# Kernel optimization log

Hardware: AMD Instinct MI355X
Metric: run time of the kernel (lower is better)

The kernel has to match this reference:

```python
import jax, jax.numpy as jnp
import numpy as np
from jax import lax

D_TEMPORAL, D_INNER, D_STATE, D_CONV, DT_RANK = 2, 4, 16, 4, 1
EPS = 1e-5


def setup_inputs() -> dict:
    key = jax.random.key(0)
    ks = jax.random.split(key, 14)
    B, L = 16, 32768
    f = lambda k, s, scale=1.0: jax.random.normal(k, s, jnp.float32) * scale
    dt_b = float(np.log(np.expm1(0.01)))  # softplus^-1(0.01), typical dt init
    A_log = jnp.log(jnp.tile(jnp.arange(1, D_STATE + 1, dtype=jnp.float32), (D_INNER, 1)))
    return {
        "hidden_states": f(ks[0], (B, D_TEMPORAL, L)),
        "norm_w": jnp.ones((D_TEMPORAL,), jnp.float32),
        "in_proj_w": f(ks[1], (2 * D_INNER, D_TEMPORAL), 0.5),
        "conv_w": f(ks[2], (D_INNER, D_CONV), 0.3),
        "conv_b": f(ks[3], (D_INNER,), 0.1),
        "x_proj_w": f(ks[4], (DT_RANK + 2 * D_STATE, D_INNER), 0.3),
        "dt_proj_w": f(ks[5], (D_INNER, DT_RANK), 1.0),
        "dt_proj_b": jnp.full((D_INNER,), dt_b, jnp.float32),
        "A_log": A_log,
        "D": jnp.ones((D_INNER,), jnp.float32),
        "conv_w_b": f(ks[6], (D_INNER, D_CONV), 0.3),
        "conv_b_b": f(ks[7], (D_INNER,), 0.1),
        "x_proj_w_b": f(ks[8], (DT_RANK + 2 * D_STATE, D_INNER), 0.3),
        "dt_proj_w_b": f(ks[9], (D_INNER, DT_RANK), 1.0),
        "dt_proj_b_b": jnp.full((D_INNER,), dt_b, jnp.float32),
        "A_b_log": A_log,
        "D_b": jnp.ones((D_INNER,), jnp.float32),
        "out_proj_w": f(ks[10], (D_TEMPORAL, D_INNER), 0.3),
        "norm_f_w": jnp.ones((D_TEMPORAL,), jnp.float32),
    }


def _silu(x):
    return x * jax.nn.sigmoid(x)


def _rmsnorm(x, w):
    return x * lax.rsqrt(jnp.mean(x * x, axis=-1, keepdims=True) + EPS) * w


def _branch(x, z, conv_w, conv_b, x_proj_w, dt_proj_w, dt_proj_b, A_log, D):
    # x, z: (B, d_inner, L). Causal depthwise conv + silu.
    Bb, d, L = x.shape
    xc = lax.conv_general_dilated(
        x, conv_w[:, None, :], (1,), [(D_CONV - 1, 0)],
        feature_group_count=d, dimension_numbers=("NCH", "OIH", "NCH"))
    u = _silu(xc + conv_b[None, :, None]).transpose(0, 2, 1)      # (B, L, d)
    x_dbl = u @ x_proj_w.T                                        # (B, L, rank+2n)
    dt, Bm, Cm = jnp.split(x_dbl, [DT_RANK, DT_RANK + D_STATE], axis=-1)
    dt = jax.nn.softplus(dt @ dt_proj_w.T + dt_proj_b)            # (B, L, d)
    A = -jnp.exp(A_log)                                           # (d, n)
    dA = jnp.exp(dt[..., None] * A)                               # (B, L, d, n)
    dBu = (dt * u)[..., None] * Bm[:, :, None, :]                 # (B, L, d, n)

    def step(h, inp):
        dA_t, dBu_t, C_t = inp
        h = dA_t * h + dBu_t                                      # (B, d, n)
        return h, jnp.einsum("bdn,bn->bd", h, C_t)

    h0 = jnp.zeros((Bb, d, D_STATE), dtype=u.dtype)
    _, ys = lax.scan(step, h0, (jnp.swapaxes(dA, 0, 1), jnp.swapaxes(dBu, 0, 1), jnp.swapaxes(Cm, 0, 1)))
    y = jnp.swapaxes(ys, 0, 1) + u * D                            # (B, L, d)
    return y * _silu(z.transpose(0, 2, 1))


def _forward(hidden_states, norm_w, in_proj_w, conv_w, conv_b, x_proj_w, dt_proj_w,
             dt_proj_b, A_log, D, conv_w_b, conv_b_b, x_proj_w_b, dt_proj_w_b,
             dt_proj_b_b, A_b_log, D_b, out_proj_w, norm_f_w):
    # hidden_states: (B, T=d_temporal, L); scan runs over L.
    hs = jnp.swapaxes(hidden_states, 1, 2)                        # (B, L, T)
    residual = hs.astype(jnp.float32)
    hs = _rmsnorm(residual, norm_w)
    xz = jnp.swapaxes(hs @ in_proj_w.T, 1, 2)                     # (B, 2*d_inner, L)
    x, z = jnp.split(xz, 2, axis=1)
    y_f = _branch(x, z, conv_w, conv_b, x_proj_w, dt_proj_w, dt_proj_b, A_log, D)
    y_b = _branch(x[..., ::-1], z[..., ::-1], conv_w_b, conv_b_b, x_proj_w_b,
                  dt_proj_w_b, dt_proj_b_b, A_b_log, D_b)
    y = y_f + y_b[:, ::-1, :]                                     # (B, L, d_inner)
    out = y @ out_proj_w.T                                        # (B, L, T)
    out = _rmsnorm(out + residual, norm_f_w)
    return jnp.swapaxes(out, 1, 2)                                # (B, T, L)


def reference(hidden_states, norm_w, in_proj_w, conv_w, conv_b, x_proj_w, dt_proj_w,
              dt_proj_b, A_log, D, conv_w_b, conv_b_b, x_proj_w_b, dt_proj_w_b,
              dt_proj_b_b, A_b_log, D_b, out_proj_w, norm_f_w):
    return _forward(hidden_states, norm_w, in_proj_w, conv_w, conv_b, x_proj_w,
                    dt_proj_w, dt_proj_b, A_log, D, conv_w_b, conv_b_b, x_proj_w_b,
                    dt_proj_w_b, dt_proj_b_b, A_b_log, D_b, out_proj_w, norm_f_w)
```

## Files before the change

### kernel.cpp

```cpp
#include <hip/hip_runtime.h>
#include <cstdint>

#define BB 16
#define LL 32768
#define NC 512
#define NSPAN 32
#define SPLEN 16
#define CPG 8

#define WD_SZ 256
#define XPW 0
#define CVW 132
#define CVB 148
#define DTW 152
#define DTB 156
#define AW  160
#define DW  224
#define G_INPROJ 512
#define G_NORMW 528
#define G_OUTP 530
#define G_NORMF 538
#define FLG 1000

#define PQ_OFF 4096
#define PQ_BYTES ((size_t)BB*2*NC*64*8)
#define SP_OFF (PQ_OFF + PQ_BYTES)
#define SP_BYTES ((size_t)BB*2*NSPAN*64*8)
#define WG_OFF (SP_OFF + SP_BYTES)
#define WG_BYTES ((size_t)BB*NC*2*64*64*2)
#define YB_OFF (WG_OFF + WG_BYTES)
#define YB_BYTES ((size_t)BB*NC*64*4*4)

#define LOG2E 1.4426950408889634f

__device__ __forceinline__ float bf2f(unsigned short u){ return __uint_as_float(((unsigned int)u)<<16); }
__device__ __forceinline__ float blo(unsigned int u){ return __uint_as_float(u<<16); }
__device__ __forceinline__ float bhi(unsigned int u){ return __uint_as_float(u & 0xffff0000u); }

__device__ __forceinline__ unsigned int cvtpk(float lo, float hi){
  unsigned int r;
  asm("v_cvt_pk_bf16_f32 %0, %1, %2" : "=v"(r) : "v"(lo), "v"(hi));
  return r;
}
__device__ __forceinline__ unsigned short cvt1(float x){
  return (unsigned short)cvtpk(x, x);
}

__device__ __forceinline__ float siluf(float x){ return x / (1.f + __expf(-x)); }
__device__ __forceinline__ float softplusf_(float x){ return fmaxf(x,0.f) + log1pf(__expf(-fabsf(x))); }

__device__ __forceinline__ float exp2fast(float x){
#if __has_builtin(__builtin_amdgcn_exp2f)
  return __builtin_amdgcn_exp2f(x);
#else
  float r; asm("v_exp_f32 %0, %1\ns_nop 0" : "=v"(r) : "v"(x)); return r;
#endif
}

__device__ __forceinline__ float rowsum16(float x){
  asm("s_nop 1\n\t"
      "v_add_f32_dpp %0, %0, %0 row_ror:1 row_mask:0xf bank_mask:0xf\n\t"
      "s_nop 1\n\t"
      "v_add_f32_dpp %0, %0, %0 row_ror:2 row_mask:0xf bank_mask:0xf\n\t"
      "s_nop 1\n\t"
      "v_add_f32_dpp %0, %0, %0 row_ror:4 row_mask:0xf bank_mask:0xf\n\t"
      "s_nop 1\n\t"
      "v_add_f32_dpp %0, %0, %0 row_ror:8 row_mask:0xf bank_mask:0xf"
      : "+v"(x));
  return x;
}

__device__ __forceinline__ float ldw(const void* p, int i, int isf){
  return isf ? ((const float*)p)[i] : bf2f(((const unsigned short*)p)[i]);
}
__device__ __forceinline__ float2 hid2(const void* hid, int isf, int b, int t){
  if (isf){
    const float* p = (const float*)hid;
    return make_float2(p[(size_t)b*2*LL + t], p[(size_t)b*2*LL + LL + t]);
  }
  const unsigned short* p = (const unsigned short*)hid;
  return make_float2(bf2f(p[(size_t)b*2*LL + t]), bf2f(p[(size_t)b*2*LL + LL + t]));
}
__device__ __forceinline__ float4 xrow(const void* __restrict__ hid, int isf,
                                       const float* __restrict__ W, int b, int t){
  float2 h = hid2(hid, isf, b, t);
  float ms = rsqrtf(0.5f*(h.x*h.x + h.y*h.y) + 1e-5f);
  float v0 = h.x*ms*W[G_NORMW], v1 = h.y*ms*W[G_NORMW+1];
  float4 x;
  x.x = W[G_INPROJ+0]*v0 + W[G_INPROJ+1]*v1;
  x.y = W[G_INPROJ+2]*v0 + W[G_INPROJ+3]*v1;
  x.z = W[G_INPROJ+4]*v0 + W[G_INPROJ+5]*v1;
  x.w = W[G_INPROJ+6]*v0 + W[G_INPROJ+7]*v1;
  return x;
}

__global__ void k_prep(const void* __restrict__ normw, const void* __restrict__ inpj,
    const void* __restrict__ cwf, const void* __restrict__ cbf,
    const void* __restrict__ xpf, const void* __restrict__ dwf,
    const void* __restrict__ dbf, const void* __restrict__ alf,
    const void* __restrict__ ddf,
    const void* __restrict__ cwb, const void* __restrict__ cbb,
    const void* __restrict__ xpb, const void* __restrict__ dwb,
    const void* __restrict__ dbb, const void* __restrict__ alb,
    const void* __restrict__ ddb,
    const void* __restrict__ outp, const void* __restrict__ nfw,
    float* __restrict__ W)
{
  const int isf = (((const unsigned int*)ddf)[0] == 0x3F800000u) ? 1 : 0;
  int t = threadIdx.x;
  for (int i=t;i<132;i+=256){ W[XPW+i]=ldw(xpf,i,isf); W[WD_SZ+XPW+i]=ldw(xpb,i,isf); }
  for (int i=t;i<16;i+=256){ W[CVW+i]=ldw(cwf,i,isf); W[WD_SZ+CVW+i]=ldw(cwb,i,isf); W[G_INPROJ+i]=ldw(inpj,i,isf); }
  for (int i=t;i<4;i+=256){
    W[CVB+i]=ldw(cbf,i,isf); W[WD_SZ+CVB+i]=ldw(cbb,i,isf);
    W[DTW+i]=ldw(dwf,i,isf); W[WD_SZ+DTW+i]=ldw(dwb,i,isf);
    W[DTB+i]=ldw(dbf,i,isf); W[WD_SZ+DTB+i]=ldw(dbb,i,isf);
    W[DW+i] =ldw(ddf,i,isf); W[WD_SZ+DW+i] =ldw(ddb,i,isf);
  }
  for (int i=t;i<64;i+=256){
    W[AW+i]       = -__expf(ldw(alf,i,isf)) * LOG2E;
    W[WD_SZ+AW+i] = -__expf(ldw(alb,i,isf)) * LOG2E;
  }
  for (int i=t;i<8;i+=256) W[G_OUTP+i]=ldw(outp,i,isf);
  for (int i=t;i<2;i+=256){ W[G_NORMW+i]=ldw(normw,i,isf); W[G_NORMF+i]=ldw(nfw,i,isf); }
  if (t==0) W[FLG] = (float)isf;
}

template<int DR>
__device__ __forceinline__ float2 scan_store(const float (* __restrict__ dtPd)[68],
    const unsigned short (* __restrict__ dtud)[68],
    const unsigned int (* __restrict__ bcd)[68],
    float (* __restrict__ ySd)[68],
    unsigned short* __restrict__ wrow,
    float Ax, int d, int n, int dn)
{
  unsigned short* wr   = wrow + dn;
  unsigned short* wrHi = wr + 32*64;
  float P = 1.f, h = 0.f;
  for (int j4=0; j4<16; j4++){
    const int t0 = DR ? 60-4*j4 : 4*j4;
    float4  d4 = *(const float4*)&dtPd[d][t0];
    ushort4 u4 = *(const ushort4*)&dtud[d][t0];
    uint4   c4 = *(const uint4*)&bcd[n][t0];
    float da[4]={d4.x,d4.y,d4.z,d4.w};
    unsigned short ua[4]={u4.x,u4.y,u4.z,u4.w};
    unsigned int ca[4]={c4.x,c4.y,c4.z,c4.w};
    float s[4];
    #pragma unroll
    for (int jr=0; jr<4; jr++){
      const int k  = DR ? 3-jr : jr;
      const int tt = t0 + k;
      float e = exp2fast(Ax*da[k]);
      P *= e;
      float Cf = bhi(ca[k]);
      h = fmaf(e, h, bf2f(ua[k])*blo(ca[k]));
      ((tt < 32) ? wr : wrHi)[(tt & 31)*64] = cvt1(P*Cf);
      s[k] = rowsum16(h*Cf);
    }
    if (n == 0) *(float4*)&ySd[d][t0] = make_float4(s[0],s[1],s[2],s[3]);
  }
  return make_float2(P, h);
}

__global__ __launch_bounds__(128, 4) void k_chunk2(const void* __restrict__ hid,
    const float* __restrict__ W, float2* __restrict__ PQ,
    unsigned short* __restrict__ Wg, float4* __restrict__ YB)
{
  __shared__ __align__(16) char smx[2176];
  __shared__ __align__(16) float dtP[2][4][68];
  __shared__ __align__(16) unsigned short dtuP[2][4][68];
  __shared__ __align__(16) unsigned int BCp[2][16][68];
  __shared__ __align__(16) float uD[2][256];
  float4* xb = (float4*)smx;
  float (*yS)[4][68] = (float (*)[4][68])smx;

  const int tid  = threadIdx.x;
  const int wid  = tid >> 6;
  const int lane = tid & 63;
  const int gid  = blockIdx.x;
  const int c    = gid & (NC-1);
  const int b    = gid >> 9;
  const int isf  = (int)W[FLG];

  if (wid == 0){
    int t = c*64 + lane;
    xb[lane+3] = xrow(hid, isf, W, b, t);
    if (lane < 3){
      int t2 = c*64 - 3 + lane;
      float4 v = make_float4(0.f,0.f,0.f,0.f);
      if (t2 >= 0) v = xrow(hid, isf, W, b, t2);
      xb[lane] = v;
    }
    if (lane >= 61){
      int t3 = c*64 + lane + 3;
      float4 v = make_float4(0.f,0.f,0.f,0.f);
      if (t3 < LL) v = xrow(hid, isf, W, b, t3);
      xb[lane+6] = v;
    }
  }
  __syncthreads();
  {
    const float* Wd = W + wid*WD_SZ;
    float4 a0,a1,a2,a3;
    if (wid == 0){ a0=xb[lane];   a1=xb[lane+1]; a2=xb[lane+2]; a3=xb[lane+3]; }
    else         { a0=xb[lane+6]; a1=xb[lane+5]; a2=xb[lane+4]; a3=xb[lane+3]; }
    float u[4];
    u[0] = siluf(Wd[CVB+0] + Wd[CVW+ 0]*a0.x + Wd[CVW+ 1]*a1.x + Wd[CVW+ 2]*a2.x + Wd[CVW+ 3]*a3.x);
    u[1] = siluf(Wd[CVB+1] + Wd[CVW+ 4]*a0.y + Wd[CVW+ 5]*a1.y + Wd[CVW+ 6]*a2.y + Wd[CVW+ 7]*a3.y);
    u[2] = siluf(Wd[CVB+2] + Wd[CVW+ 8]*a0.z + Wd[CVW+ 9]*a1.z + Wd[CVW+10]*a2.z + Wd[CVW+11]*a3.z);
    u[3] = siluf(Wd[CVB+3] + Wd[CVW+12]*a0.w + Wd[CVW+13]*a1.w + Wd[CVW+14]*a2.w + Wd[CVW+15]*a3.w);
    float dtr = Wd[XPW+0]*u[0] + Wd[XPW+1]*u[1] + Wd[XPW+2]*u[2] + Wd[XPW+3]*u[3];
    float4 ud4;
    #pragma unroll
    for (int d2=0; d2<4; d2++){
      float dt = softplusf_(fmaf(Wd[DTW+d2], dtr, Wd[DTB+d2]));
      dtP[wid][d2][lane]  = dt;
      dtuP[wid][d2][lane] = cvt1(dt*u[d2]);
      ((float*)&ud4)[d2] = u[d2]*Wd[DW+d2];
    }
    *(float4*)&uD[wid][lane*4] = ud4;
    #pragma unroll
    for (int n=0; n<16; n++){
      float Bn = Wd[XPW+(1+n)*4+0]*u[0] + Wd[XPW+(1+n)*4+1]*u[1]
               + Wd[XPW+(1+n)*4+2]*u[2] + Wd[XPW+(1+n)*4+3]*u[3];
      float Cn = Wd[XPW+(17+n)*4+0]*u[0] + Wd[XPW+(17+n)*4+1]*u[1]
               + Wd[XPW+(17+n)*4+2]*u[2] + Wd[XPW+(17+n)*4+3]*u[3];
      BCp[wid][n][lane] = cvtpk(Bn, Cn);
    }
  }
  __syncthreads();

  const int d = lane>>4, n = lane&15;
  const float Ax = W[wid*WD_SZ + AW + d*16 + n];
  unsigned short* wrow = Wg + ((size_t)gid*2 + wid)*64*64;
  float2 pq;
  size_t idx;
  if (wid == 0){
    pq  = scan_store<0>(dtP[0], dtuP[0], BCp[0], yS[0], wrow, Ax, d, n, lane);
    idx = ((size_t)(b*2+0)*NC + c);
  } else {
    pq  = scan_store<1>(dtP[1], dtuP[1], BCp[1], yS[1], wrow, Ax, d, n, lane);
    idx = ((size_t)(b*2+1)*NC + (NC-1-c));
  }
  PQ[idx*64 + lane] = pq;
  __syncthreads();

  if (wid == 0){
    float4 v;
    v.x = yS[0][0][lane] + yS[1][0][lane] + uD[0][lane*4+0] + uD[1][lane*4+0];
    v.y = yS[0][1][lane] + yS[1][1][lane] + uD[0][lane*4+1] + uD[1][lane*4+1];
    v.z = yS[0][2][lane] + yS[1][2][lane] + uD[0][lane*4+2] + uD[1][lane*4+2];
    v.w = yS[0][3][lane] + yS[1][3][lane] + uD[0][lane*4+3] + uD[1][lane*4+3];
    YB[(size_t)gid*64 + lane] = v;
  }
}

__global__ __launch_bounds__(64) void k_spans(const float2* __restrict__ PQ,
                                              float2* __restrict__ SP)
{
  const int blk  = blockIdx.x;
  const int lane = threadIdx.x;
  const int bd   = blk >> 5, span = blk & (NSPAN-1);
  const float2* p = PQ + ((size_t)bd*NC + span*SPLEN)*64 + lane;
  float2 v[SPLEN];
  #pragma unroll
  for (int k=0;k<SPLEN;k++) v[k] = p[k*64];
  float A = 1.f, Bc = 0.f;
  #pragma unroll
  for (int k=0;k<SPLEN;k++){ A *= v[k].x; Bc = fmaf(v[k].x, Bc, v[k].y); }
  SP[((size_t)bd*NSPAN + span)*64 + lane] = make_float2(A,Bc);
}

__device__ __forceinline__ float dot16(uint4 q0, uint4 q1, const float* h){
  float4 h0 = *(const float4*)(h+0),  h1 = *(const float4*)(h+4);
  float4 h2 = *(const float4*)(h+8),  h3 = *(const float4*)(h+12);
  float cacc = 0.f;
  cacc = fmaf(blo(q0.x), h0.x, cacc); cacc = fmaf(bhi(q0.x), h0.y, cacc);
  cacc = fmaf(blo(q0.y), h0.z, cacc); cacc = fmaf(bhi(q0.y), h0.w, cacc);
  cacc = fmaf(blo(q0.z), h1.x, cacc); cacc = fmaf(bhi(q0.z), h1.y, cacc);
  cacc = fmaf(blo(q0.w), h1.z, cacc); cacc = fmaf(bhi(q0.w), h1.w, cacc);
  cacc = fmaf(blo(q1.x), h2.x, cacc); cacc = fmaf(bhi(q1.x), h2.y, cacc);
  cacc = fmaf(blo(q1.y), h2.z, cacc); cacc = fmaf(bhi(q1.y), h2.w, cacc);
  cacc = fmaf(blo(q1.z), h3.x, cacc); cacc = fmaf(bhi(q1.z), h3.y, cacc);
  cacc = fmaf(blo(q1.w), h3.z, cacc); cacc = fmaf(bhi(q1.w), h3.w, cacc);
  return cacc;
}

__device__ __forceinline__ float compose_h0(const float2* __restrict__ PQ,
    const float2* __restrict__ SP, int bd, int p, int lane)
{
  const int s  = p >> 4, wn = p & 15;
  const float2* SPb = SP + (size_t)bd*NSPAN*64 + lane;
  const float2* PQb = PQ + ((size_t)bd*NC + (p & ~15))*64 + lane;
  float h = 0.f;
  #pragma unroll
  for (int jg=0; jg<4; jg++){
    if (jg*8 < s){
      float2 v[8];
      #pragma unroll
      for (int j=0;j<8;j++){ int jj = jg*8+j; v[j] = SPb[(size_t)(jj<s?jj:0)*64]; }
      #pragma unroll
      for (int j=0;j<8;j++){ int jj = jg*8+j; if (jj<s) h = fmaf(v[j].x, h, v[j].y); }
    }
  }
  #pragma unroll
  for (int jg=0; jg<2; jg++){
    if (jg*8 < wn){
      float2 v[8];
      #pragma unroll
      for (int j=0;j<8;j++){ int jj = jg*8+j; v[j] = PQb[(size_t)(jj<wn?jj:0)*64]; }
      #pragma unroll
      for (int j=0;j<8;j++){ int jj = jg*8+j; if (jj<wn) h = fmaf(v[j].x, h, v[j].y); }
    }
  }
  return h;
}

#define WROW 72
__global__ __launch_bounds__(128, 2) void k_final(const void* __restrict__ hid,
    const float* __restrict__ W, const float2* __restrict__ PQ,
    const float2* __restrict__ SP, const unsigned short* __restrict__ Wg,
    const float4* __restrict__ YB, void* __restrict__ out)
{
  __shared__ __align__(16) unsigned short Wt[2][64][WROW];
  __shared__ __align__(16) float yC[2][CPG][64][4];
  __shared__ __align__(16) float h0s[2][64];
  const int tid  = threadIdx.x;
  const int wid  = tid >> 6;
  const int lane = tid & 63;
  const int gb   = blockIdx.x;
  const int b    = gb >> 6;
  const int c0   = (gb & 63) * CPG;
  const int isf  = (int)W[FLG];
  const int bd   = b*2 + wid;

  const int i_first = wid ? (CPG-1) : 0;
  const int c_first = c0 + i_first;
  const int p_first = wid ? (NC-1-c_first) : c_first;

  const uint4* gt0 = (const uint4*)(Wg + ((size_t)(b*NC + c_first)*2 + wid)*64*64);
  uint4 st[8];
  #pragma unroll
  for (int k2=0;k2<8;k2++) st[k2] = gt0[k2*64 + lane];

  float h = compose_h0(PQ, SP, bd, p_first, lane);

  #pragma unroll
  for (int k2=0;k2<8;k2++){
    int j = k2*64 + lane;
    *(uint4*)&Wt[wid][j>>3][(j&7)*8] = st[k2];
  }

  const float2* PQd = PQ + (size_t)bd*NC*64 + lane;

  for (int step=0; step<CPG; ++step){
    const int i_cur = wid ? (CPG-1-step) : step;
    const int c_cur = c0 + i_cur;
    const int hasN  = (step < CPG-1);
    const int i_nxt = wid ? (i_cur-1) : (i_cur+1);

    uint4 sn[8];
    if (hasN){
      const uint4* g2 = (const uint4*)(Wg + ((size_t)(b*NC + c0 + i_nxt)*2 + wid)*64*64);
      #pragma unroll
      for (int k2=0;k2<8;k2++) sn[k2] = g2[k2*64 + lane];
    }

    h0s[wid][lane] = h;

    {
      uint4 wr_[8];
      #pragma unroll
      for (int q=0;q<8;q++) wr_[q] = *(const uint4*)&Wt[wid][lane][q*8];
      float4 cr;
      #pragma unroll
      for (int d2=0; d2<4; d2++)
        ((float*)&cr)[d2] = dot16(wr_[d2*2], wr_[d2*2+1], &h0s[wid][d2*16]);
      *(float4*)&yC[wid][i_cur][lane][0] = cr;
    }

    if (hasN){
      const int q = wid ? (NC-1-c_cur) : c_cur;
      float2 pq = PQd[(size_t)q*64];
      h = fmaf(pq.x, h, pq.y);
      #pragma unroll
      for (int k2=0;k2<8;k2++){
        int j = k2*64 + lane;
        *(uint4*)&Wt[wid][j>>3][(j&7)*8] = sn[k2];
      }
    }
  }
  __syncthreads();

  #pragma unroll
  for (int ii=0; ii<CPG/2; ii++){
    const int i  = wid*(CPG/2) + ii;
    const int c  = c0 + i;
    const int t  = lane;
    const int tg = c*64 + t;
    float4 cF = *(const float4*)&yC[0][i][t][0];
    float4 cB = *(const float4*)&yC[1][i][t][0];
    float4 yb = YB[(size_t)(b*NC + c)*64 + t];

    float2 r = hid2(hid, isf, b, tg);
    float ms0 = rsqrtf(0.5f*(r.x*r.x + r.y*r.y) + 1e-5f);
    float v0 = r.x*ms0*W[G_NORMW], v1 = r.y*ms0*W[G_NORMW+1];
    float z0 = siluf(W[G_INPROJ+ 8]*v0 + W[G_INPROJ+ 9]*v1);
    float z1 = siluf(W[G_INPROJ+10]*v0 + W[G_INPROJ+11]*v1);
    float z2 = siluf(W[G_INPROJ+12]*v0 + W[G_INPROJ+13]*v1);
    float z3 = siluf(W[G_INPROJ+14]*v0 + W[G_INPROJ+15]*v1);

    float y0 = (yb.x + cF.x + cB.x) * z0;
    float y1 = (yb.y + cF.y + cB.y) * z1;
    float y2 = (yb.z + cF.z + cB.z) * z2;
    float y3 = (yb.w + cF.w + cB.w) * z3;
    float o0 = W[G_OUTP+0]*y0 + W[G_OUTP+1]*y1 + W[G_OUTP+2]*y2 + W[G_OUTP+3]*y3;
    float o1 = W[G_OUTP+4]*y0 + W[G_OUTP+5]*y1 + W[G_OUTP+6]*y2 + W[G_OUTP+7]*y3;
    o0 += r.x;
    o1 += r.y;
    float ms = rsqrtf(0.5f*(o0*o0 + o1*o1) + 1e-5f);
    float e0 = o0*ms*W[G_NORMF], e1 = o1*ms*W[G_NORMF+1];
    size_t i0 = (size_t)b*2*LL + tg, i1 = i0 + LL;
    if (isf){
      ((float*)out)[i0] = e0;
      ((float*)out)[i1] = e1;
    } else {
      ((unsigned short*)out)[i0] = cvt1(e0);
      ((unsigned short*)out)[i1] = cvt1(e1);
    }
  }
}

extern "C" void kernel_launch(void* const* d_in, const int* in_sizes, int n_in,
                              void* d_out, int out_size, void* d_ws, size_t ws_size,
                              hipStream_t stream)
{
  (void)in_sizes; (void)n_in; (void)out_size; (void)ws_size;
  const void* hid   = d_in[0];
  const void* normw = d_in[1];
  const void* inpj  = d_in[2];
  const void* cwf   = d_in[3];
  const void* cbf   = d_in[4];
  const void* xpf   = d_in[5];
  const void* dwf   = d_in[6];
  const void* dbf   = d_in[7];
  const void* alf   = d_in[8];
  const void* ddf   = d_in[9];
  const void* cwb   = d_in[10];
  const void* cbb   = d_in[11];
  const void* xpb   = d_in[12];
  const void* dwb   = d_in[13];
  const void* dbb   = d_in[14];
  const void* alb   = d_in[15];
  const void* ddb   = d_in[16];
  const void* outp  = d_in[17];
  const void* nfw   = d_in[18];

  float* W            = (float*)d_ws;
  float2* PQ          = (float2*)((char*)d_ws + PQ_OFF);
  float2* SPt         = (float2*)((char*)d_ws + SP_OFF);
  unsigned short* Wg  = (unsigned short*)((char*)d_ws + WG_OFF);
  float4* YB          = (float4*)((char*)d_ws + YB_OFF);

  k_prep<<<1,256,0,stream>>>(normw, inpj, cwf, cbf, xpf, dwf, dbf, alf, ddf,
                             cwb, cbb, xpb, dwb, dbb, alb, ddb, outp, nfw, W);
  k_chunk2<<<BB*NC, 128, 0, stream>>>(hid, W, PQ, Wg, YB);
  k_spans<<<BB*2*NSPAN, 64, 0, stream>>>(PQ, SPt);
  k_final<<<BB*(NC/CPG), 128, 0, stream>>>(hid, W, PQ, SPt, Wg, YB, d_out);
}
```

Measured before the change: 181.5 us.

## Split final stage into atomic correction kernel and separate output kernel

Replaces k_final with two kernels. k_corr runs one 64-thread block per direction and chunk group (CPG reduced to 4) and adds the carried-state corrections straight into YB with atomicAdd. k_out then applies gating, out_proj and the final RMSNorm per element. The aim is more parallel blocks and less serial chaining per block, at the cost of an extra launch, global float atomics and another pass over YB. dt*u is also kept in float instead of bf16 in shared memory, and the halo load in k_chunk2 is simplified.

```diff
diff --git a/kernel.cpp b/kernel.cpp
--- a/kernel.cpp
+++ b/kernel.cpp
@@ -6,7 +6,7 @@
 #define NC 512
 #define NSPAN 32
 #define SPLEN 16
-#define CPG 8
+#define CPG 4
 
 #define WD_SZ 256
 #define XPW 0
@@ -127,7 +127,7 @@
 
 template<int DR>
 __device__ __forceinline__ float2 scan_store(const float (* __restrict__ dtPd)[68],
-    const unsigned short (* __restrict__ dtud)[68],
+    const float (* __restrict__ dtud)[68],
     const unsigned int (* __restrict__ bcd)[68],
     float (* __restrict__ ySd)[68],
     unsigned short* __restrict__ wrow,
@@ -139,10 +139,10 @@
   for (int j4=0; j4<16; j4++){
     const int t0 = DR ? 60-4*j4 : 4*j4;
     float4  d4 = *(const float4*)&dtPd[d][t0];
-    ushort4 u4 = *(const ushort4*)&dtud[d][t0];
+    float4  u4 = *(const float4*)&dtud[d][t0];
     uint4   c4 = *(const uint4*)&bcd[n][t0];
     float da[4]={d4.x,d4.y,d4.z,d4.w};
-    unsigned short ua[4]={u4.x,u4.y,u4.z,u4.w};
+    float ua[4]={u4.x,u4.y,u4.z,u4.w};
     unsigned int ca[4]={c4.x,c4.y,c4.z,c4.w};
     float s[4];
     #pragma unroll
@@ -152,7 +152,7 @@
       float e = exp2fast(Ax*da[k]);
       P *= e;
       float Cf = bhi(ca[k]);
-      h = fmaf(e, h, bf2f(ua[k])*blo(ca[k]));
+      h = fmaf(e, h, ua[k]*blo(ca[k]));
       ((tt < 32) ? wr : wrHi)[(tt & 31)*64] = cvt1(P*Cf);
       s[k] = rowsum16(h*Cf);
     }
@@ -167,7 +167,7 @@
 {
   __shared__ __align__(16) char smx[2176];
   __shared__ __align__(16) float dtP[2][4][68];
-  __shared__ __align__(16) unsigned short dtuP[2][4][68];
+  __shared__ __align__(16) float dtuP[2][4][68];
   __shared__ __align__(16) unsigned int BCp[2][16][68];
   __shared__ __align__(16) float uD[2][256];
   float4* xb = (float4*)smx;
@@ -181,21 +181,11 @@
   const int b    = gid >> 9;
   const int isf  = (int)W[FLG];
 
-  if (wid == 0){
-    int t = c*64 + lane;
-    xb[lane+3] = xrow(hid, isf, W, b, t);
-    if (lane < 3){
-      int t2 = c*64 - 3 + lane;
-      float4 v = make_float4(0.f,0.f,0.f,0.f);
-      if (t2 >= 0) v = xrow(hid, isf, W, b, t2);
-      xb[lane] = v;
-    }
-    if (lane >= 61){
-      int t3 = c*64 + lane + 3;
-      float4 v = make_float4(0.f,0.f,0.f,0.f);
-      if (t3 < LL) v = xrow(hid, isf, W, b, t3);
-      xb[lane+6] = v;
-    }
+  if (tid < 70){
+    int t2 = c*64 - 3 + tid;
+    float4 v = make_float4(0.f,0.f,0.f,0.f);
+    if (t2 >= 0 && t2 < LL) v = xrow(hid, isf, W, b, t2);
+    xb[tid] = v;
   }
   __syncthreads();
   {
@@ -214,7 +204,7 @@
     for (int d2=0; d2<4; d2++){
       float dt = softplusf_(fmaf(Wd[DTW+d2], dtr, Wd[DTB+d2]));
       dtP[wid][d2][lane]  = dt;
-      dtuP[wid][d2][lane] = cvt1(dt*u[d2]);
+      dtuP[wid][d2][lane] = dt*u[d2];
       ((float*)&ud4)[d2] = u[d2]*Wd[DW+d2];
     }
     *(float4*)&uD[wid][lane*4] = ud4;
@@ -316,28 +306,23 @@
 }
 
 #define WROW 72
-__global__ __launch_bounds__(128, 2) void k_final(const void* __restrict__ hid,
-    const float* __restrict__ W, const float2* __restrict__ PQ,
-    const float2* __restrict__ SP, const unsigned short* __restrict__ Wg,
-    const float4* __restrict__ YB, void* __restrict__ out)
-{
-  __shared__ __align__(16) unsigned short Wt[2][64][WROW];
-  __shared__ __align__(16) float yC[2][CPG][64][4];
-  __shared__ __align__(16) float h0s[2][64];
-  const int tid  = threadIdx.x;
-  const int wid  = tid >> 6;
-  const int lane = tid & 63;
-  const int gb   = blockIdx.x;
-  const int b    = gb >> 6;
-  const int c0   = (gb & 63) * CPG;
-  const int isf  = (int)W[FLG];
-  const int bd   = b*2 + wid;
-
-  const int i_first = wid ? (CPG-1) : 0;
-  const int c_first = c0 + i_first;
-  const int p_first = wid ? (NC-1-c_first) : c_first;
-
-  const uint4* gt0 = (const uint4*)(Wg + ((size_t)(b*NC + c_first)*2 + wid)*64*64);
+__global__ __launch_bounds__(64) void k_corr(
+    const float2* __restrict__ PQ, const float2* __restrict__ SP,
+    const unsigned short* __restrict__ Wg, float* __restrict__ YBf)
+{
+  __shared__ __align__(16) unsigned short Wt[64][WROW];
+  __shared__ float h0s[64];
+  const int lane = threadIdx.x;
+  const int gid  = blockIdx.x;
+  const int g    = gid & 127;
+  const int bd   = gid >> 7;
+  const int dir  = bd & 1;
+  const int b    = bd >> 1;
+
+  const int c_first = dir ? g*CPG + CPG-1 : g*CPG;
+  const int p_first = dir ? (NC-1-c_first) : c_first;
+
+  const uint4* gt0 = (const uint4*)(Wg + ((size_t)(b*NC + c_first)*2 + dir)*64*64);
   uint4 st[8];
   #pragma unroll
   for (int k2=0;k2<8;k2++) st[k2] = gt0[k2*64 + lane];
@@ -347,86 +332,85 @@
   #pragma unroll
   for (int k2=0;k2<8;k2++){
     int j = k2*64 + lane;
-    *(uint4*)&Wt[wid][j>>3][(j&7)*8] = st[k2];
+    *(uint4*)&Wt[j>>3][(j&7)*8] = st[k2];
   }
 
   const float2* PQd = PQ + (size_t)bd*NC*64 + lane;
-
   for (int step=0; step<CPG; ++step){
-    const int i_cur = wid ? (CPG-1-step) : step;
-    const int c_cur = c0 + i_cur;
+    const int i_cur = dir ? (CPG-1-step) : step;
+    const int c_cur = g*CPG + i_cur;
     const int hasN  = (step < CPG-1);
-    const int i_nxt = wid ? (i_cur-1) : (i_cur+1);
 
     uint4 sn[8];
     if (hasN){
-      const uint4* g2 = (const uint4*)(Wg + ((size_t)(b*NC + c0 + i_nxt)*2 + wid)*64*64);
+      const int c_nxt = dir ? (c_cur-1) : (c_cur+1);
+      const uint4* g2 = (const uint4*)(Wg + ((size_t)(b*NC + c_nxt)*2 + dir)*64*64);
       #pragma unroll
       for (int k2=0;k2<8;k2++) sn[k2] = g2[k2*64 + lane];
     }
 
-    h0s[wid][lane] = h;
-
-    {
-      uint4 wr_[8];
-      #pragma unroll
-      for (int q=0;q<8;q++) wr_[q] = *(const uint4*)&Wt[wid][lane][q*8];
-      float4 cr;
-      #pragma unroll
-      for (int d2=0; d2<4; d2++)
-        ((float*)&cr)[d2] = dot16(wr_[d2*2], wr_[d2*2+1], &h0s[wid][d2*16]);
-      *(float4*)&yC[wid][i_cur][lane][0] = cr;
-    }
+    h0s[lane] = h;
+
+    uint4 wr_[8];
+    #pragma unroll
+    for (int q=0;q<8;q++) wr_[q] = *(const uint4*)&Wt[lane][q*8];
+    float cr[4];
+    #pragma unroll
+    for (int d2=0; d2<4; d2++)
+      cr[d2] = dot16(wr_[d2*2], wr_[d2*2+1], &h0s[d2*16]);
+
+    float* yb = YBf + ((size_t)(b*NC + c_cur)*64 + lane)*4;
+    #pragma unroll
+    for (int d2=0; d2<4; d2++) atomicAdd(yb + d2, cr[d2]);
 
     if (hasN){
-      const int q = wid ? (NC-1-c_cur) : c_cur;
-      float2 pq = PQd[(size_t)q*64];
+      const int p_cur = dir ? (NC-1-c_cur) : c_cur;
+      float2 pq = PQd[(size_t)p_cur*64];
       h = fmaf(pq.x, h, pq.y);
       #pragma unroll
       for (int k2=0;k2<8;k2++){
         int j = k2*64 + lane;
-        *(uint4*)&Wt[wid][j>>3][(j&7)*8] = sn[k2];
+        *(uint4*)&Wt[j>>3][(j&7)*8] = sn[k2];
       }
     }
   }
-  __syncthreads();
-
-  #pragma unroll
-  for (int ii=0; ii<CPG/2; ii++){
-    const int i  = wid*(CPG/2) + ii;
-    const int c  = c0 + i;
-    const int t  = lane;
-    const int tg = c*64 + t;
-    float4 cF = *(const float4*)&yC[0][i][t][0];
-    float4 cB = *(const float4*)&yC[1][i][t][0];
-    float4 yb = YB[(size_t)(b*NC + c)*64 + t];
-
-    float2 r = hid2(hid, isf, b, tg);
-    float ms0 = rsqrtf(0.5f*(r.x*r.x + r.y*r.y) + 1e-5f);
-    float v0 = r.x*ms0*W[G_NORMW], v1 = r.y*ms0*W[G_NORMW+1];
-    float z0 = siluf(W[G_INPROJ+ 8]*v0 + W[G_INPROJ+ 9]*v1);
-    float z1 = siluf(W[G_INPROJ+10]*v0 + W[G_INPROJ+11]*v1);
-    float z2 = siluf(W[G_INPROJ+12]*v0 + W[G_INPROJ+13]*v1);
-    float z3 = siluf(W[G_INPROJ+14]*v0 + W[G_INPROJ+15]*v1);
-
-    float y0 = (yb.x + cF.x + cB.x) * z0;
-    float y1 = (yb.y + cF.y + cB.y) * z1;
-    float y2 = (yb.z + cF.z + cB.z) * z2;
-    float y3 = (yb.w + cF.w + cB.w) * z3;
-    float o0 = W[G_OUTP+0]*y0 + W[G_OUTP+1]*y1 + W[G_OUTP+2]*y2 + W[G_OUTP+3]*y3;
-    float o1 = W[G_OUTP+4]*y0 + W[G_OUTP+5]*y1 + W[G_OUTP+6]*y2 + W[G_OUTP+7]*y3;
-    o0 += r.x;
-    o1 += r.y;
-    float ms = rsqrtf(0.5f*(o0*o0 + o1*o1) + 1e-5f);
-    float e0 = o0*ms*W[G_NORMF], e1 = o1*ms*W[G_NORMF+1];
-    size_t i0 = (size_t)b*2*LL + tg, i1 = i0 + LL;
-    if (isf){
-      ((float*)out)[i0] = e0;
-      ((float*)out)[i1] = e1;
-    } else {
-      ((unsigned short*)out)[i0] = cvt1(e0);
-      ((unsigned short*)out)[i1] = cvt1(e1);
-    }
+}
+
+__global__ __launch_bounds__(256) void k_out(const void* __restrict__ hid,
+    const float* __restrict__ W, const float4* __restrict__ YB,
+    void* __restrict__ out)
+{
+  const int gidx = blockIdx.x*256 + threadIdx.x;
+  const int b = gidx >> 15;
+  const int t = gidx & (LL-1);
+  const int isf = (int)W[FLG];
+
+  float4 y4 = YB[(size_t)b*LL + t];
+  float2 r = hid2(hid, isf, b, t);
+  float ms0 = rsqrtf(0.5f*(r.x*r.x + r.y*r.y) + 1e-5f);
+  float v0 = r.x*ms0*W[G_NORMW], v1 = r.y*ms0*W[G_NORMW+1];
+  float z0 = siluf(W[G_INPROJ+ 8]*v0 + W[G_INPROJ+ 9]*v1);
+  float z1 = siluf(W[G_INPROJ+10]*v0 + W[G_INPROJ+11]*v1);
+  float z2 = siluf(W[G_INPROJ+12]*v0 + W[G_INPROJ+13]*v1);
+  float z3 = siluf(W[G_INPROJ+14]*v0 + W[G_INPROJ+15]*v1);
+
+  float y0 = y4.x * z0;
+  float y1 = y4.y * z1;
+  float y2 = y4.z * z2;
+  float y3 = y4.w * z3;
+  float o0 = W[G_OUTP+0]*y0 + W[G_OUTP+1]*y1 + W[G_OUTP+2]*y2 + W[G_OUTP+3]*y3;
+  float o1 = W[G_OUTP+4]*y0 + W[G_OUTP+5]*y1 + W[G_OUTP+6]*y2 + W[G_OUTP+7]*y3;
+  o0 += r.x;
+  o1 += r.y;
+  float ms = rsqrtf(0.5f*(o0*o0 + o1*o1) + 1e-5f);
+  float e0 = o0*ms*W[G_NORMF], e1 = o1*ms*W[G_NORMF+1];
+  size_t i0 = (size_t)b*2*LL + t, i1 = i0 + LL;
+  if (isf){
+    ((float*)out)[i0] = e0;
+    ((float*)out)[i1] = e1;
+  } else {
+    ((unsigned short*)out)[i0] = cvt1(e0);
+    ((unsigned short*)out)[i1] = cvt1(e1);
   }
 }
 
@@ -465,5 +449,6 @@
                              cwb, cbb, xpb, dwb, dbb, alb, ddb, outp, nfw, W);
   k_chunk2<<<BB*NC, 128, 0, stream>>>(hid, W, PQ, Wg, YB);
   k_spans<<<BB*2*NSPAN, 64, 0, stream>>>(PQ, SPt);
-  k_final<<<BB*(NC/CPG), 128, 0, stream>>>(hid, W, PQ, SPt, Wg, YB, d_out);
-}
+  k_corr<<<BB*2*(NC/CPG), 64, 0, stream>>>(PQ, SPt, Wg, (float*)YB);
+  k_out<<<(BB*LL)/256, 256, 0, stream>>>(hid, W, YB, d_out);
+}
```

Measured after the change: 223.2 us. 1.23x slower.

## Replace materialized bf16 decay-weight matrix with dt prefix sums and C recomputation

Applied to the files above, without the earlier changes.

Before, the chunk kernel wrote a 64x64 bf16 matrix of cumulative-decay times C weights per chunk and direction, and the final kernel read it back. Now the chunk kernel stores only a wave-level inclusive prefix sum of dt per channel and the packed bf16 C vector per timestep. The final kernel rebuilds exp2(A*cumdt) on the fly, and the chunk decay P comes from the total dt sum. This removes most of the workspace traffic and the LDS tile staging, allowing higher occupancy for k_final, at the cost of many extra exp2 evaluations per step and a different rounding path (dt*u is now kept in fp32).

```diff
diff --git a/kernel.cpp b/kernel.cpp
--- a/kernel.cpp
+++ b/kernel.cpp
@@ -26,9 +26,11 @@
 #define PQ_BYTES ((size_t)BB*2*NC*64*8)
 #define SP_OFF (PQ_OFF + PQ_BYTES)
 #define SP_BYTES ((size_t)BB*2*NSPAN*64*8)
-#define WG_OFF (SP_OFF + SP_BYTES)
-#define WG_BYTES ((size_t)BB*NC*2*64*64*2)
-#define YB_OFF (WG_OFF + WG_BYTES)
+#define SG_OFF (SP_OFF + SP_BYTES)
+#define SG_BYTES ((size_t)BB*NC*2*64*4*4)
+#define CG_OFF (SG_OFF + SG_BYTES)
+#define CG_BYTES ((size_t)BB*NC*2*64*16*2)
+#define YB_OFF (CG_OFF + CG_BYTES)
 #define YB_BYTES ((size_t)BB*NC*64*4*4)
 
 #define LOG2E 1.4426950408889634f
@@ -70,6 +72,22 @@
   return x;
 }
 
+__device__ __forceinline__ float wavescan_incl(float x){
+  union { float f; int i; } a, t;
+  a.f = x;
+  t.i = __builtin_amdgcn_update_dpp(0, a.i, 0x111, 0xf, 0xf, true); a.f += t.f;
+  t.i = __builtin_amdgcn_update_dpp(0, a.i, 0x112, 0xf, 0xf, true); a.f += t.f;
+  t.i = __builtin_amdgcn_update_dpp(0, a.i, 0x114, 0xf, 0xf, true); a.f += t.f;
+  t.i = __builtin_amdgcn_update_dpp(0, a.i, 0x118, 0xf, 0xf, true); a.f += t.f;
+  t.i = __builtin_amdgcn_update_dpp(0, a.i, 0x142, 0xa, 0xf, true); a.f += t.f;
+  t.i = __builtin_amdgcn_update_dpp(0, a.i, 0x143, 0xc, 0xf, true); a.f += t.f;
+  return a.f;
+}
+__device__ __forceinline__ float readlane63(float x){
+  union { float f; int i; } a; a.f = x;
+  return __uint_as_float((unsigned)__builtin_amdgcn_readlane(a.i, 63));
+}
+
 __device__ __forceinline__ float ldw(const void* p, int i, int isf){
   return isf ? ((const float*)p)[i] : bf2f(((const unsigned short*)p)[i]);
 }
@@ -126,50 +144,45 @@
 }
 
 template<int DR>
-__device__ __forceinline__ float2 scan_store(const float (* __restrict__ dtPd)[68],
-    const unsigned short (* __restrict__ dtud)[68],
+__device__ __forceinline__ float scan_local(const float (* __restrict__ dtPd)[68],
+    const float (* __restrict__ dtud)[68],
     const unsigned int (* __restrict__ bcd)[68],
     float (* __restrict__ ySd)[68],
-    unsigned short* __restrict__ wrow,
-    float Ax, int d, int n, int dn)
-{
-  unsigned short* wr   = wrow + dn;
-  unsigned short* wrHi = wr + 32*64;
-  float P = 1.f, h = 0.f;
+    float Ax, int d, int n)
+{
+  float h = 0.f;
   for (int j4=0; j4<16; j4++){
     const int t0 = DR ? 60-4*j4 : 4*j4;
     float4  d4 = *(const float4*)&dtPd[d][t0];
-    ushort4 u4 = *(const ushort4*)&dtud[d][t0];
+    float4  u4 = *(const float4*)&dtud[d][t0];
     uint4   c4 = *(const uint4*)&bcd[n][t0];
     float da[4]={d4.x,d4.y,d4.z,d4.w};
-    unsigned short ua[4]={u4.x,u4.y,u4.z,u4.w};
+    float ua[4]={u4.x,u4.y,u4.z,u4.w};
     unsigned int ca[4]={c4.x,c4.y,c4.z,c4.w};
     float s[4];
     #pragma unroll
     for (int jr=0; jr<4; jr++){
       const int k  = DR ? 3-jr : jr;
-      const int tt = t0 + k;
       float e = exp2fast(Ax*da[k]);
-      P *= e;
-      float Cf = bhi(ca[k]);
-      h = fmaf(e, h, bf2f(ua[k])*blo(ca[k]));
-      ((tt < 32) ? wr : wrHi)[(tt & 31)*64] = cvt1(P*Cf);
-      s[k] = rowsum16(h*Cf);
+      h = fmaf(e, h, ua[k]*blo(ca[k]));
+      s[k] = rowsum16(h*bhi(ca[k]));
     }
     if (n == 0) *(float4*)&ySd[d][t0] = make_float4(s[0],s[1],s[2],s[3]);
   }
-  return make_float2(P, h);
+  return h;
 }
 
 __global__ __launch_bounds__(128, 4) void k_chunk2(const void* __restrict__ hid,
     const float* __restrict__ W, float2* __restrict__ PQ,
-    unsigned short* __restrict__ Wg, float4* __restrict__ YB)
+    float* __restrict__ sG, unsigned int* __restrict__ Cg,
+    float4* __restrict__ YB)
 {
   __shared__ __align__(16) char smx[2176];
   __shared__ __align__(16) float dtP[2][4][68];
-  __shared__ __align__(16) unsigned short dtuP[2][4][68];
+  __shared__ __align__(16) float dtuP[2][4][68];
   __shared__ __align__(16) unsigned int BCp[2][16][68];
   __shared__ __align__(16) float uD[2][256];
+  __shared__ float sTot[2][4];
   float4* xb = (float4*)smx;
   float (*yS)[4][68] = (float (*)[4][68])smx;
 
@@ -180,22 +193,13 @@
   const int c    = gid & (NC-1);
   const int b    = gid >> 9;
   const int isf  = (int)W[FLG];
-
-  if (wid == 0){
-    int t = c*64 + lane;
-    xb[lane+3] = xrow(hid, isf, W, b, t);
-    if (lane < 3){
-      int t2 = c*64 - 3 + lane;
-      float4 v = make_float4(0.f,0.f,0.f,0.f);
-      if (t2 >= 0) v = xrow(hid, isf, W, b, t2);
-      xb[lane] = v;
-    }
-    if (lane >= 61){
-      int t3 = c*64 + lane + 3;
-      float4 v = make_float4(0.f,0.f,0.f,0.f);
-      if (t3 < LL) v = xrow(hid, isf, W, b, t3);
-      xb[lane+6] = v;
-    }
+  const size_t cd = (size_t)gid*2 + wid;
+
+  if (tid < 70){
+    int t2 = c*64 - 3 + tid;
+    float4 v = make_float4(0.f,0.f,0.f,0.f);
+    if (t2 >= 0 && t2 < LL) v = xrow(hid, isf, W, b, t2);
+    xb[tid] = v;
   }
   __syncthreads();
   {
@@ -214,10 +218,11 @@
     for (int d2=0; d2<4; d2++){
       float dt = softplusf_(fmaf(Wd[DTW+d2], dtr, Wd[DTB+d2]));
       dtP[wid][d2][lane]  = dt;
-      dtuP[wid][d2][lane] = cvt1(dt*u[d2]);
+      dtuP[wid][d2][lane] = dt*u[d2];
       ((float*)&ud4)[d2] = u[d2]*Wd[DW+d2];
     }
     *(float4*)&uD[wid][lane*4] = ud4;
+    float Cl[16];
     #pragma unroll
     for (int n=0; n<16; n++){
       float Bn = Wd[XPW+(1+n)*4+0]*u[0] + Wd[XPW+(1+n)*4+1]*u[1]
@@ -225,23 +230,44 @@
       float Cn = Wd[XPW+(17+n)*4+0]*u[0] + Wd[XPW+(17+n)*4+1]*u[1]
                + Wd[XPW+(17+n)*4+2]*u[2] + Wd[XPW+(17+n)*4+3]*u[3];
       BCp[wid][n][lane] = cvtpk(Bn, Cn);
-    }
+      Cl[n] = Cn;
+    }
+    unsigned int cp[8];
+    #pragma unroll
+    for (int q=0;q<8;q++) cp[q] = cvtpk(Cl[2*q], Cl[2*q+1]);
+    uint4* cgw = (uint4*)(Cg + cd*512);
+    cgw[lane*2+0] = *(uint4*)&cp[0];
+    cgw[lane*2+1] = *(uint4*)&cp[4];
   }
   __syncthreads();
+
+  {
+    float sv[4], tt[4];
+    #pragma unroll
+    for (int d2=0; d2<4; d2++){
+      float v = dtP[wid][d2][lane];
+      float x = wavescan_incl(v);
+      float tot = readlane63(x);
+      if (wid) x = tot - x + v;
+      sv[d2] = x; tt[d2] = tot;
+    }
+    *(float4*)(sG + cd*256 + lane*4) = make_float4(sv[0],sv[1],sv[2],sv[3]);
+    if (lane == 0){ sTot[wid][0]=tt[0]; sTot[wid][1]=tt[1]; sTot[wid][2]=tt[2]; sTot[wid][3]=tt[3]; }
+  }
 
   const int d = lane>>4, n = lane&15;
   const float Ax = W[wid*WD_SZ + AW + d*16 + n];
-  unsigned short* wrow = Wg + ((size_t)gid*2 + wid)*64*64;
-  float2 pq;
+  float h;
   size_t idx;
   if (wid == 0){
-    pq  = scan_store<0>(dtP[0], dtuP[0], BCp[0], yS[0], wrow, Ax, d, n, lane);
+    h   = scan_local<0>(dtP[0], dtuP[0], BCp[0], yS[0], Ax, d, n);
     idx = ((size_t)(b*2+0)*NC + c);
   } else {
-    pq  = scan_store<1>(dtP[1], dtuP[1], BCp[1], yS[1], wrow, Ax, d, n, lane);
+    h   = scan_local<1>(dtP[1], dtuP[1], BCp[1], yS[1], Ax, d, n);
     idx = ((size_t)(b*2+1)*NC + (NC-1-c));
   }
-  PQ[idx*64 + lane] = pq;
+  float P = exp2fast(Ax * sTot[wid][d]);
+  PQ[idx*64 + lane] = make_float2(P, h);
   __syncthreads();
 
   if (wid == 0){
@@ -268,21 +294,6 @@
   #pragma unroll
   for (int k=0;k<SPLEN;k++){ A *= v[k].x; Bc = fmaf(v[k].x, Bc, v[k].y); }
   SP[((size_t)bd*NSPAN + span)*64 + lane] = make_float2(A,Bc);
-}
-
-__device__ __forceinline__ float dot16(uint4 q0, uint4 q1, const float* h){
-  float4 h0 = *(const float4*)(h+0),  h1 = *(const float4*)(h+4);
-  float4 h2 = *(const float4*)(h+8),  h3 = *(const float4*)(h+12);
-  float cacc = 0.f;
-  cacc = fmaf(blo(q0.x), h0.x, cacc); cacc = fmaf(bhi(q0.x), h0.y, cacc);
-  cacc = fmaf(blo(q0.y), h0.z, cacc); cacc = fmaf(bhi(q0.y), h0.w, cacc);
-  cacc = fmaf(blo(q0.z), h1.x, cacc); cacc = fmaf(bhi(q0.z), h1.y, cacc);
-  cacc = fmaf(blo(q0.w), h1.z, cacc); cacc = fmaf(bhi(q0.w), h1.w, cacc);
-  cacc = fmaf(blo(q1.x), h2.x, cacc); cacc = fmaf(bhi(q1.x), h2.y, cacc);
-  cacc = fmaf(blo(q1.y), h2.z, cacc); cacc = fmaf(bhi(q1.y), h2.w, cacc);
-  cacc = fmaf(blo(q1.z), h3.x, cacc); cacc = fmaf(bhi(q1.z), h3.y, cacc);
-  cacc = fmaf(blo(q1.w), h3.z, cacc); cacc = fmaf(bhi(q1.w), h3.w, cacc);
-  return cacc;
 }
 
 __device__ __forceinline__ float compose_h0(const float2* __restrict__ PQ,
@@ -315,15 +326,15 @@
   return h;
 }
 
-#define WROW 72
-__global__ __launch_bounds__(128, 2) void k_final(const void* __restrict__ hid,
+__global__ __launch_bounds__(128, 4) void k_final(const void* __restrict__ hid,
     const float* __restrict__ W, const float2* __restrict__ PQ,
-    const float2* __restrict__ SP, const unsigned short* __restrict__ Wg,
-    const float4* __restrict__ YB, void* __restrict__ out)
-{
-  __shared__ __align__(16) unsigned short Wt[2][64][WROW];
-  __shared__ __align__(16) float yC[2][CPG][64][4];
-  __shared__ __align__(16) float h0s[2][64];
+    const float2* __restrict__ SP, const float* __restrict__ sG,
+    const unsigned int* __restrict__ Cg, const float4* __restrict__ YB,
+    void* __restrict__ out)
+{
+  __shared__ float h0s[2][64];
+  __shared__ float As[2][64];
+  __shared__ __align__(16) float4 yC[2][CPG][64];
   const int tid  = threadIdx.x;
   const int wid  = tid >> 6;
   const int lane = tid & 63;
@@ -333,60 +344,66 @@
   const int isf  = (int)W[FLG];
   const int bd   = b*2 + wid;
 
+  As[wid][lane] = W[wid*WD_SZ + AW + lane];
+
   const int i_first = wid ? (CPG-1) : 0;
   const int c_first = c0 + i_first;
   const int p_first = wid ? (NC-1-c_first) : c_first;
 
-  const uint4* gt0 = (const uint4*)(Wg + ((size_t)(b*NC + c_first)*2 + wid)*64*64);
-  uint4 st[8];
-  #pragma unroll
-  for (int k2=0;k2<8;k2++) st[k2] = gt0[k2*64 + lane];
+  size_t cdf = ((size_t)(b*NC + c_first)*2 + wid);
+  float4 s4 = *(const float4*)(sG + cdf*256 + lane*4);
+  uint4 c8a = ((const uint4*)(Cg + cdf*512))[lane*2+0];
+  uint4 c8b = ((const uint4*)(Cg + cdf*512))[lane*2+1];
 
   float h = compose_h0(PQ, SP, bd, p_first, lane);
-
-  #pragma unroll
-  for (int k2=0;k2<8;k2++){
-    int j = k2*64 + lane;
-    *(uint4*)&Wt[wid][j>>3][(j&7)*8] = st[k2];
-  }
-
   const float2* PQd = PQ + (size_t)bd*NC*64 + lane;
 
   for (int step=0; step<CPG; ++step){
     const int i_cur = wid ? (CPG-1-step) : step;
     const int c_cur = c0 + i_cur;
     const int hasN  = (step < CPG-1);
-    const int i_nxt = wid ? (i_cur-1) : (i_cur+1);
-
-    uint4 sn[8];
+
+    float4 s4n; uint4 can, cbn;
     if (hasN){
-      const uint4* g2 = (const uint4*)(Wg + ((size_t)(b*NC + c0 + i_nxt)*2 + wid)*64*64);
+      const int c_nxt = wid ? (c_cur-1) : (c_cur+1);
+      size_t cdn = ((size_t)(b*NC + c_nxt)*2 + wid);
+      s4n = *(const float4*)(sG + cdn*256 + lane*4);
+      can = ((const uint4*)(Cg + cdn*512))[lane*2+0];
+      cbn = ((const uint4*)(Cg + cdn*512))[lane*2+1];
+    }
+
+    h0s[wid][lane] = h;
+
+    float cf[16];
+    cf[ 0]=blo(c8a.x); cf[ 1]=bhi(c8a.x); cf[ 2]=blo(c8a.y); cf[ 3]=bhi(c8a.y);
+    cf[ 4]=blo(c8a.z); cf[ 5]=bhi(c8a.z); cf[ 6]=blo(c8a.w); cf[ 7]=bhi(c8a.w);
+    cf[ 8]=blo(c8b.x); cf[ 9]=bhi(c8b.x); cf[10]=blo(c8b.y); cf[11]=bhi(c8b.y);
+    cf[12]=blo(c8b.z); cf[13]=bhi(c8b.z); cf[14]=blo(c8b.w); cf[15]=bhi(c8b.w);
+
+    float4 cr;
+    #pragma unroll
+    for (int d2=0; d2<4; d2++){
+      float sd = ((const float*)&s4)[d2];
+      const float4* Af = (const float4*)&As[wid][d2*16];
+      const float4* Hf = (const float4*)&h0s[wid][d2*16];
+      float acc = 0.f;
       #pragma unroll
-      for (int k2=0;k2<8;k2++) sn[k2] = g2[k2*64 + lane];
-    }
-
-    h0s[wid][lane] = h;
-
-    {
-      uint4 wr_[8];
-      #pragma unroll
-      for (int q=0;q<8;q++) wr_[q] = *(const uint4*)&Wt[wid][lane][q*8];
-      float4 cr;
-      #pragma unroll
-      for (int d2=0; d2<4; d2++)
-        ((float*)&cr)[d2] = dot16(wr_[d2*2], wr_[d2*2+1], &h0s[wid][d2*16]);
-      *(float4*)&yC[wid][i_cur][lane][0] = cr;
-    }
+      for (int q=0;q<4;q++){
+        float4 a4 = Af[q]; float4 h4 = Hf[q];
+        acc = fmaf(exp2fast(a4.x*sd), cf[q*4+0]*h4.x, acc);
+        acc = fmaf(exp2fast(a4.y*sd), cf[q*4+1]*h4.y, acc);
+        acc = fmaf(exp2fast(a4.z*sd), cf[q*4+2]*h4.z, acc);
+        acc = fmaf(exp2fast(a4.w*sd), cf[q*4+3]*h4.w, acc);
+      }
+      ((float*)&cr)[d2] = acc;
+    }
+    yC[wid][i_cur][lane] = cr;
 
     if (hasN){
-      const int q = wid ? (NC-1-c_cur) : c_cur;
-      float2 pq = PQd[(size_t)q*64];
+      const int p_cur = wid ? (NC-1-c_cur) : c_cur;
+      float2 pq = PQd[(size_t)p_cur*64];
       h = fmaf(pq.x, h, pq.y);
-      #pragma unroll
-      for (int k2=0;k2<8;k2++){
-        int j = k2*64 + lane;
-        *(uint4*)&Wt[wid][j>>3][(j&7)*8] = sn[k2];
-      }
+      s4 = s4n; c8a = can; c8b = cbn;
     }
   }
   __syncthreads();
@@ -397,8 +414,8 @@
     const int c  = c0 + i;
     const int t  = lane;
     const int tg = c*64 + t;
-    float4 cF = *(const float4*)&yC[0][i][t][0];
-    float4 cB = *(const float4*)&yC[1][i][t][0];
+    float4 cF = yC[0][i][t];
+    float4 cB = yC[1][i][t];
     float4 yb = YB[(size_t)(b*NC + c)*64 + t];
 
     float2 r = hid2(hid, isf, b, tg);
@@ -458,12 +475,13 @@
   float* W            = (float*)d_ws;
   float2* PQ          = (float2*)((char*)d_ws + PQ_OFF);
   float2* SPt         = (float2*)((char*)d_ws + SP_OFF);
-  unsigned short* Wg  = (unsigned short*)((char*)d_ws + WG_OFF);
+  float* sG           = (float*)((char*)d_ws + SG_OFF);
+  unsigned int* Cg    = (unsigned int*)((char*)d_ws + CG_OFF);
   float4* YB          = (float4*)((char*)d_ws + YB_OFF);
 
   k_prep<<<1,256,0,stream>>>(normw, inpj, cwf, cbf, xpf, dwf, dbf, alf, ddf,
                              cwb, cbb, xpb, dwb, dbb, alb, ddb, outp, nfw, W);
-  k_chunk2<<<BB*NC, 128, 0, stream>>>(hid, W, PQ, Wg, YB);
+  k_chunk2<<<BB*NC, 128, 0, stream>>>(hid, W, PQ, sG, Cg, YB);
   k_spans<<<BB*2*NSPAN, 64, 0, stream>>>(PQ, SPt);
-  k_final<<<BB*(NC/CPG), 128, 0, stream>>>(hid, W, PQ, SPt, Wg, YB, d_out);
-}
+  k_final<<<BB*(NC/CPG), 128, 0, stream>>>(hid, W, PQ, SPt, sG, Cg, YB, d_out);
+}
```

Measured after the change: 185.1 us. About the same (+2.0%).
